# Performance work log

Hardware: AMD Instinct MI355X
Metric: run time of the kernel (lower is better)

Reference implementation:

```python
import jax, jax.numpy as jnp
import numpy as np

L, H, DK, DV, DM, DH = 6, 12, 64, 64, 768, 3072
B, T = 8, 1024


def pos_embed(T, N, dtype):
    pos = jnp.arange(T, dtype=jnp.float32)[:, None]
    i = jnp.arange(N)[None, :]
    exp = ((i // 2) * 2).astype(jnp.float32) / N
    ang = pos / jnp.power(jnp.float32(10000.0), exp)
    pe = jnp.where(i % 2 == 0, jnp.sin(ang), jnp.cos(ang))
    return pe.astype(dtype)


def layernorm(x, g, b, eps=1e-5):
    mu = jnp.mean(x, axis=-1, keepdims=True)
    var = jnp.mean((x - mu) ** 2, axis=-1, keepdims=True)
    return (x - mu) * jax.lax.rsqrt(var + eps) * g + b


def setup_inputs() -> dict:
    key = jax.random.key(0)
    ks = jax.random.split(key, 16)
    s = 0.02
    return {
        "x": jax.random.normal(ks[0], (B, T, DM), dtype=jnp.float32),
        "mask": jnp.ones((B, T), dtype=bool),
        "wq": jax.random.normal(ks[1], (L, H, DM, DK), dtype=jnp.float32) * s,
        "wk": jax.random.normal(ks[2], (L, H, DM, DK), dtype=jnp.float32) * s,
        "wv": jax.random.normal(ks[3], (L, H, DM, DV), dtype=jnp.float32) * s,
        "proj_w": jax.random.normal(ks[4], (L, H * DV, DM), dtype=jnp.float32) * s,
        "proj_b": jnp.zeros((L, DM), dtype=jnp.float32),
        "ln1_g": jnp.ones((L, DM), dtype=jnp.float32),
        "ln1_b": jnp.zeros((L, DM), dtype=jnp.float32),
        "w1": jax.random.normal(ks[5], (L, DM, DH), dtype=jnp.float32) * s,
        "b1": jnp.zeros((L, DH), dtype=jnp.float32),
        "w2": jax.random.normal(ks[6], (L, DH, DM), dtype=jnp.float32) * s,
        "b2": jnp.zeros((L, DM), dtype=jnp.float32),
        "ln2_g": jnp.ones((L, DM), dtype=jnp.float32),
        "ln2_b": jnp.zeros((L, DM), dtype=jnp.float32),
    }


def reference(x, mask, wq, wk, wv, proj_w, proj_b, ln1_g, ln1_b, w1, b1, w2, b2, ln2_g, ln2_b):
    Bx, Tx, Dm = x.shape
    nlayers = wq.shape[0]
    x = x + pos_embed(Tx, Dm, x.dtype)  # sinusoidal PE, added in-place in original
    m = mask[:, None, None, :]          # [B,1,1,Tk], broadcast over heads and queries
    scale = Dm ** 0.5                   # NOTE: original divides by sqrt(Dm), not sqrt(Dk)
    for l in range(nlayers):
        q = jnp.einsum('btd,hdk->bhtk', x, wq[l])
        k = jnp.einsum('bsd,hdk->bhsk', x, wk[l])
        v = jnp.einsum('bsd,hdv->bhsv', x, wv[l])
        attn = jnp.einsum('bhtk,bhsk->bhts', q, k) / scale
        attn = jnp.where(m, attn, -jnp.inf)
        p = jax.nn.softmax(attn, axis=-1)
        o = jnp.einsum('bhts,bhsv->bhtv', p, v)
        o = o.transpose(0, 2, 1, 3).reshape(Bx, Tx, -1)  # concat heads: [B,T,H*Dv]
        o = o @ proj_w[l] + proj_b[l]
        x = layernorm(o + x, ln1_g[l], ln1_b[l])
        h = jax.nn.relu(x @ w1[l] + b1[l])
        f = h @ w2[l] + b2[l]
        x = layernorm(f + x, ln2_g[l], ln2_b[l])
    return x
```

## Files before the change

### kernel.cpp

```cpp
#include <hip/hip_runtime.h>
#include <hip/hip_bf16.h>
#include <math.h>

constexpr int LAYERS = 6;
constexpr int HEADS  = 12;
constexpr int DK     = 64;
constexpr int DM     = 768;
constexpr int DH     = 3072;
constexpr int BATCH  = 8;
constexpr int SEQ    = 1024;
constexpr int MROWS  = BATCH * SEQ;
constexpr float QSCALE = 0.03608439182435161f * 1.4426950408889634f;

typedef __attribute__((ext_vector_type(4))) float f32x4;
typedef __attribute__((ext_vector_type(8))) short bf16x8;
typedef __attribute__((ext_vector_type(4))) unsigned short u16x4;

enum { EPI_QKV = 0, EPI_PROJ = 1, EPI_RELU = 2, EPI_FFN2 = 3 };

__device__ __forceinline__ void gload_lds16(const void* g, void* l) {
  __builtin_amdgcn_global_load_lds(
      (const __attribute__((address_space(1))) void*)g,
      (__attribute__((address_space(3))) void*)l, 16, 0, 0);
}

__global__ __launch_bounds__(256) void posembed_kernel(
    const float* __restrict__ x, float* __restrict__ x_cur,
    __hip_bfloat16* __restrict__ xb) {
  int idx = blockIdx.x * 256 + threadIdx.x;
  int d  = idx % DM;
  int bt = idx / DM;
  int t  = bt & (SEQ - 1);
  float expo = (float)(d & ~1) * (1.0f / (float)DM);
  float inv  = powf(10000.0f, -expo);
  float ang  = (float)t * inv;
  float pe   = (d & 1) ? cosf(ang) : sinf(ang);
  float v = x[idx] + pe;
  x_cur[idx] = v;
  xb[idx] = __float2bfloat16(v);
}

__global__ __launch_bounds__(256) void transpose_conv(
    const float* __restrict__ in, __hip_bfloat16* __restrict__ out,
    int R, int C, long obatch) {
  __shared__ float tile[32][33];
  int batch = blockIdx.z;
  in  += (long)batch * R * C;
  out += (long)batch * obatch;
  int c0 = blockIdx.x * 32, r0 = blockIdx.y * 32;
  int tx = threadIdx.x, ty = threadIdx.y;
  for (int i = 0; i < 4; i++) {
    int r = r0 + ty + i * 8;
    tile[ty + i * 8][tx] = in[(long)r * C + c0 + tx];
  }
  __syncthreads();
  for (int i = 0; i < 4; i++) {
    int oc = ty + i * 8;
    out[(long)(c0 + oc) * R + r0 + tx] = __float2bfloat16(tile[tx][oc]);
  }
}

__global__ __launch_bounds__(256) void qkv_transpose(
    const float* __restrict__ wq, const float* __restrict__ wk,
    const float* __restrict__ wv, __hip_bfloat16* __restrict__ out) {
  __shared__ float tile[32][33];
  const int z = blockIdx.z;
  const int which = z / 12, head = z % 12;
  const float* in = (which == 0 ? wq : which == 1 ? wk : wv)
                    + (size_t)head * DM * DK;
  __hip_bfloat16* o = out + (size_t)which * DM * DM + (size_t)head * DK * DM;
  int c0 = blockIdx.x * 32, r0 = blockIdx.y * 32;
  int tx = threadIdx.x, ty = threadIdx.y;
  for (int i = 0; i < 4; i++) {
    int r = r0 + ty + i * 8;
    tile[ty + i * 8][tx] = in[(long)r * DK + c0 + tx];
  }
  __syncthreads();
  for (int i = 0; i < 4; i++) {
    int oc = ty + i * 8;
    o[(long)(c0 + oc) * DM + r0 + tx] = __float2bfloat16(tile[tx][oc]);
  }
}

__global__ __launch_bounds__(256) void vtrans_kernel(
    const __hip_bfloat16* __restrict__ v, __hip_bfloat16* __restrict__ vt) {
  __shared__ unsigned short tile[64][66];
  const int head = blockIdx.y;
  const int t0 = blockIdx.x * 64;
  const unsigned short* src =
      (const unsigned short*)v + (size_t)head * SEQ * DK + (size_t)t0 * DK;
  unsigned short* dst = (unsigned short*)vt + (size_t)head * SEQ * DK + t0;
  const int tid = threadIdx.x;
#pragma unroll
  for (int it = 0; it < 4; ++it) {
    int j = tid + it * 256;
    int r = j >> 4;
    int c4 = (j & 15) * 4;
    u16x4 d4 = *(const u16x4*)&src[(size_t)r * DK + c4];
    tile[r][c4 + 0] = d4[0]; tile[r][c4 + 1] = d4[1];
    tile[r][c4 + 2] = d4[2]; tile[r][c4 + 3] = d4[3];
  }
  __syncthreads();
#pragma unroll
  for (int it = 0; it < 4; ++it) {
    int j = tid + it * 256;
    int d = j >> 4;
    int t4 = (j & 15) * 4;
    u16x4 o4;
    o4[0] = tile[t4 + 0][d]; o4[1] = tile[t4 + 1][d];
    o4[2] = tile[t4 + 2][d]; o4[3] = tile[t4 + 3][d];
    *(u16x4*)&dst[(size_t)d * SEQ + t4] = o4;
  }
}

template <int EPI>
__global__ __launch_bounds__(256, 2) void gemm_bt(
    const __hip_bfloat16* __restrict__ A,
    const __hip_bfloat16* __restrict__ BT,
    int K,
    const float* __restrict__ bias,
    const float* __restrict__ res,
    void* __restrict__ outp) {
  __shared__ __align__(16) __hip_bfloat16 As[128 * 32];
  __shared__ __align__(16) __hip_bfloat16 Bs[128 * 32];
  const int m0 = blockIdx.y * 128;
  const int n0 = blockIdx.x * 128;
  const int tid = threadIdx.x;
  const int lane = tid & 63;
  const int w = tid >> 6;
  const int wm = w >> 1, wn = w & 1;
  const int g = lane >> 4, r16 = lane & 15;

  f32x4 acc[4][4] = {};

  const int srow = tid >> 2;
  const int scol = (tid & 3) * 8;
  const __hip_bfloat16* aS = A + (size_t)(m0 + srow) * K + scol;
  const __hip_bfloat16* bS = BT + (size_t)(n0 + srow) * K + scol;

  for (int k0 = 0; k0 < K; k0 += 32) {
    __syncthreads();
    gload_lds16(aS + k0,          &As[tid * 8]);
    gload_lds16(aS + 64 * K + k0, &As[2048 + tid * 8]);
    gload_lds16(bS + k0,          &Bs[tid * 8]);
    gload_lds16(bS + 64 * K + k0, &Bs[2048 + tid * 8]);
    __syncthreads();

    bf16x8 af[4], bfr[4];
#pragma unroll
    for (int m = 0; m < 4; m++)
      af[m] = *(const bf16x8*)&As[(wm * 64 + m * 16 + r16) * 32 + g * 8];
#pragma unroll
    for (int n = 0; n < 4; n++)
      bfr[n] = *(const bf16x8*)&Bs[(wn * 64 + n * 16 + r16) * 32 + g * 8];
#pragma unroll
    for (int m = 0; m < 4; m++)
#pragma unroll
      for (int n = 0; n < 4; n++)
        acc[m][n] = __builtin_amdgcn_mfma_f32_16x16x32_bf16(
            af[m], bfr[n], acc[m][n], 0, 0, 0);
  }

#pragma unroll
  for (int m = 0; m < 4; m++)
#pragma unroll
    for (int n = 0; n < 4; n++)
#pragma unroll
      for (int r = 0; r < 4; r++) {
        int row = m0 + wm * 64 + m * 16 + g * 4 + r;
        int col = n0 + wn * 64 + n * 16 + r16;
        float v = acc[m][n][r];
        if (EPI == EPI_QKV) {
          int which = (col >= 2 * DM) ? 2 : (col >= DM ? 1 : 0);
          int hc = col - which * DM;
          int h = hc >> 6, dk = hc & 63;
          int b = row >> 10, t = row & (SEQ - 1);
          if (which == 0) v *= QSCALE;
          ((__hip_bfloat16*)outp)[(((size_t)(which * BATCH + b) * HEADS + h) * SEQ + t) * DK + dk] =
              __float2bfloat16(v);
        } else if (EPI == EPI_PROJ || EPI == EPI_FFN2) {
          ((float*)outp)[(size_t)row * DM + col] =
              v + bias[col] + res[(size_t)row * DM + col];
        } else {
          v += bias[col];
          ((__hip_bfloat16*)outp)[(size_t)row * DH + col] =
              __float2bfloat16(v > 0.f ? v : 0.f);
        }
      }
}

__global__ __launch_bounds__(256, 4) void flash_kernel(
    const __hip_bfloat16* __restrict__ qkv,
    const __hip_bfloat16* __restrict__ vt,
    __hip_bfloat16* __restrict__ obuf) {
  __shared__ __align__(16) char KL[2][8192];
  __shared__ __align__(16) char VL[2][8192];
  __shared__ __align__(16) char PsL[4][2048];

  const int bid = blockIdx.x;
  const int qb = bid / 96;
  const int bh = bid % 96;
  const int h = bh % HEADS, b = bh / HEADS;

  const int tid = threadIdx.x, lane = tid & 63, w = tid >> 6;
  const int g = lane >> 4, r16 = lane & 15;
  const int r7 = r16 & 7;

  const size_t headoff = ((size_t)b * HEADS + h) * SEQ * DK;
  const size_t planes = (size_t)BATCH * HEADS * SEQ * DK;
  const __hip_bfloat16* Q  = qkv + headoff;
  const __hip_bfloat16* Kg = qkv + planes + headoff;
  const __hip_bfloat16* Vg = vt + headoff;

  bf16x8 qf[2];
  {
    int qrow = qb * 64 + w * 16 + r16;
    qf[0] = *(const bf16x8*)&Q[(size_t)qrow * DK + g * 8];
    qf[1] = *(const bf16x8*)&Q[(size_t)qrow * DK + 32 + g * 8];
  }

  f32x4 o_acc[4] = {};
  float m_run = -3e38f;
  float lsum[4] = {0.f, 0.f, 0.f, 0.f};

  const int s0j = tid, s1j = tid + 256;
  const int s0r = s0j >> 3, s0c = (s0j & 7) ^ (s0r & 7);
  const int s1r = s1j >> 3, s1c = (s1j & 7) ^ (s1r & 7);

  auto stage = [&](int tt, int d) {
    const int ss = tt * 64;
    gload_lds16(&Kg[(size_t)(ss + s0r) * DK + s0c * 8], &KL[d][s0j * 16]);
    gload_lds16(&Kg[(size_t)(ss + s1r) * DK + s1c * 8], &KL[d][s1j * 16]);
    gload_lds16(&Vg[(size_t)s0r * SEQ + ss + s0c * 8], &VL[d][s0j * 16]);
    gload_lds16(&Vg[(size_t)s1r * SEQ + ss + s1c * 8], &VL[d][s1j * 16]);
  };

  stage(0, 0);
  __syncthreads();

  for (int t = 0; t < SEQ / 64; ++t) {
    const int cur = t & 1;
    if (t < SEQ / 64 - 1) stage(t + 1, cur ^ 1);

    f32x4 s_acc[4] = {};
#pragma unroll
    for (int n = 0; n < 4; ++n) {
      const int R = n * 16 + r16;
      bf16x8 k0 = *(const bf16x8*)&KL[cur][R * 128 + ((g ^ r7) << 4)];
      s_acc[n] = __builtin_amdgcn_mfma_f32_16x16x32_bf16(qf[0], k0, s_acc[n], 0, 0, 0);
      bf16x8 k1 = *(const bf16x8*)&KL[cur][R * 128 + (((4 + g) ^ r7) << 4)];
      s_acc[n] = __builtin_amdgcn_mfma_f32_16x16x32_bf16(qf[1], k1, s_acc[n], 0, 0, 0);
    }

    float mx = -3e38f;
#pragma unroll
    for (int n = 0; n < 4; ++n)
      mx = fmaxf(mx, fmaxf(fmaxf(s_acc[n][0], s_acc[n][1]),
                           fmaxf(s_acc[n][2], s_acc[n][3])));
#pragma unroll
    for (int off = 1; off < 16; off <<= 1) mx = fmaxf(mx, __shfl_xor(mx, off, 64));

    if (__any(mx > m_run + 8.f)) {
      float mnew = fmaxf(m_run, mx);
      float alpha = exp2f(m_run - mnew);
      m_run = mnew;
#pragma unroll
      for (int r = 0; r < 4; ++r) lsum[r] *= alpha;
#pragma unroll
      for (int n = 0; n < 4; ++n)
#pragma unroll
        for (int r = 0; r < 4; ++r) o_acc[n][r] *= alpha;
    }

    char* Pw = &PsL[w][0];
#pragma unroll
    for (int n = 0; n < 4; ++n)
#pragma unroll
      for (int r = 0; r < 4; ++r) {
        float p = exp2f(s_acc[n][r] - m_run);
        lsum[r] += p;
        int trow = g * 4 + r;
        int chunk = n * 2 + (r16 >> 3);
        *(unsigned short*)&Pw[trow * 128 + ((chunk * 16) ^ ((trow & 7) << 4)) + r7 * 2] =
            __bfloat16_as_ushort(__float2bfloat16(p));
      }

    asm volatile("s_waitcnt lgkmcnt(0)" ::: "memory");
    __builtin_amdgcn_s_barrier();
    __builtin_amdgcn_sched_barrier(0);

#pragma unroll
    for (int kk = 0; kk < 2; ++kk) {
      bf16x8 pf = *(const bf16x8*)&Pw[r16 * 128 + (((kk * 4 + g) * 16) ^ (r7 << 4))];
#pragma unroll
      for (int n = 0; n < 4; ++n) {
        bf16x8 vf = *(const bf16x8*)&VL[cur][(n * 16 + r16) * 128 +
                                            (((kk * 4 + g) ^ r7) << 4)];
        o_acc[n] = __builtin_amdgcn_mfma_f32_16x16x32_bf16(pf, vf, o_acc[n], 0, 0, 0);
      }
    }

    asm volatile("s_waitcnt vmcnt(0)" ::: "memory");
    __builtin_amdgcn_s_barrier();
    __builtin_amdgcn_sched_barrier(0);
  }

#pragma unroll
  for (int r = 0; r < 4; ++r)
#pragma unroll
    for (int off = 1; off < 16; off <<= 1) lsum[r] += __shfl_xor(lsum[r], off, 64);
  float rinv[4];
#pragma unroll
  for (int r = 0; r < 4; ++r) rinv[r] = 1.0f / lsum[r];

#pragma unroll
  for (int n = 0; n < 4; ++n)
#pragma unroll
    for (int r = 0; r < 4; ++r) {
      int t = qb * 64 + w * 16 + g * 4 + r;
      int col = h * DK + n * 16 + r16;
      obuf[((size_t)b * SEQ + t) * DM + col] =
          __float2bfloat16(o_acc[n][r] * rinv[r]);
    }
}

__global__ __launch_bounds__(256) void ln_kernel(
    const float* __restrict__ y, const float* __restrict__ gam,
    const float* __restrict__ bet, float* __restrict__ xout,
    __hip_bfloat16* __restrict__ xb) {
  int row = blockIdx.x;
  const float* yr = y + (size_t)row * DM;
  int tid = threadIdx.x;
  float v[3];
  float s1 = 0.f, s2 = 0.f;
#pragma unroll
  for (int i = 0; i < 3; i++) {
    v[i] = yr[tid + i * 256];
    s1 += v[i];
    s2 += v[i] * v[i];
  }
#pragma unroll
  for (int off = 1; off < 64; off <<= 1) {
    s1 += __shfl_xor(s1, off, 64);
    s2 += __shfl_xor(s2, off, 64);
  }
  __shared__ float ps1[4], ps2[4];
  int w = tid >> 6;
  if ((tid & 63) == 0) { ps1[w] = s1; ps2[w] = s2; }
  __syncthreads();
  s1 = ps1[0] + ps1[1] + ps1[2] + ps1[3];
  s2 = ps2[0] + ps2[1] + ps2[2] + ps2[3];
  float mu = s1 * (1.f / DM);
  float var = s2 * (1.f / DM) - mu * mu;
  float rstd = rsqrtf(var + 1e-5f);
#pragma unroll
  for (int i = 0; i < 3; i++) {
    int d = tid + i * 256;
    float o = (v[i] - mu) * rstd * gam[d] + bet[d];
    xout[(size_t)row * DM + d] = o;
    xb[(size_t)row * DM + d] = __float2bfloat16(o);
  }
}

extern "C" void kernel_launch(void* const* d_in, const int* in_sizes, int n_in,
                              void* d_out, int out_size, void* d_ws, size_t ws_size,
                              hipStream_t stream) {
  const float* x_in   = (const float*)d_in[0];
  const float* wq     = (const float*)d_in[2];
  const float* wk     = (const float*)d_in[3];
  const float* wv     = (const float*)d_in[4];
  const float* proj_w = (const float*)d_in[5];
  const float* proj_b = (const float*)d_in[6];
  const float* ln1_g  = (const float*)d_in[7];
  const float* ln1_b  = (const float*)d_in[8];
  const float* w1     = (const float*)d_in[9];
  const float* b1     = (const float*)d_in[10];
  const float* w2     = (const float*)d_in[11];
  const float* b2     = (const float*)d_in[12];
  const float* ln2_g  = (const float*)d_in[13];
  const float* ln2_b  = (const float*)d_in[14];

  size_t off = 0;
  auto alloc = [&](size_t bytes) {
    void* p = (char*)d_ws + off;
    off += (bytes + 255) & ~(size_t)255;
    return p;
  };
  float* x_cur = (float*)alloc((size_t)MROWS * DM * 4);
  __hip_bfloat16* xb    = (__hip_bfloat16*)alloc((size_t)MROWS * DM * 2);
  __hip_bfloat16* qkvb  = (__hip_bfloat16*)alloc((size_t)3 * MROWS * DM * 2);
  __hip_bfloat16* obuf  = (__hip_bfloat16*)alloc((size_t)MROWS * DM * 2);
  float* ybuf  = (float*)alloc((size_t)MROWS * DM * 4);
  __hip_bfloat16* hbuf  = (__hip_bfloat16*)alloc((size_t)MROWS * DH * 2);
  __hip_bfloat16* qkvt  = (__hip_bfloat16*)alloc((size_t)3 * DM * DM * 2);
  __hip_bfloat16* projt = (__hip_bfloat16*)alloc((size_t)DM * DM * 2);
  __hip_bfloat16* w1t   = (__hip_bfloat16*)alloc((size_t)DH * DM * 2);
  __hip_bfloat16* w2t   = (__hip_bfloat16*)alloc((size_t)DM * DH * 2);
  __hip_bfloat16* vtb   = hbuf;

  posembed_kernel<<<MROWS * DM / 256, 256, 0, stream>>>(x_in, x_cur, xb);

  for (int l = 0; l < LAYERS; l++) {
    qkv_transpose<<<dim3(2, 24, 36), dim3(32, 8), 0, stream>>>(
        wq + (size_t)l * HEADS * DM * DK, wk + (size_t)l * HEADS * DM * DK,
        wv + (size_t)l * HEADS * DM * DK, qkvt);
    transpose_conv<<<dim3(24, 24, 1), dim3(32, 8), 0, stream>>>(
        proj_w + (size_t)l * DM * DM, projt, DM, DM, 0);
    transpose_conv<<<dim3(96, 24, 1), dim3(32, 8), 0, stream>>>(
        w1 + (size_t)l * DM * DH, w1t, DM, DH, 0);
    transpose_conv<<<dim3(24, 96, 1), dim3(32, 8), 0, stream>>>(
        w2 + (size_t)l * DH * DM, w2t, DH, DM, 0);

    gemm_bt<EPI_QKV><<<dim3(18, 64), 256, 0, stream>>>(
        xb, qkvt, DM, nullptr, nullptr, qkvb);
    vtrans_kernel<<<dim3(16, 96), 256, 0, stream>>>(
        qkvb + (size_t)2 * MROWS * DM, vtb);
    flash_kernel<<<dim3((SEQ / 64) * HEADS * BATCH), 256, 0, stream>>>(
        qkvb, vtb, obuf);
    gemm_bt<EPI_PROJ><<<dim3(6, 64), 256, 0, stream>>>(
        obuf, projt, DM, proj_b + (size_t)l * DM, x_cur, ybuf);
    ln_kernel<<<MROWS, 256, 0, stream>>>(
        ybuf, ln1_g + (size_t)l * DM, ln1_b + (size_t)l * DM, x_cur, xb);
    gemm_bt<EPI_RELU><<<dim3(24, 64), 256, 0, stream>>>(
        xb, w1t, DM, b1 + (size_t)l * DH, nullptr, hbuf);
    gemm_bt<EPI_FFN2><<<dim3(6, 64), 256, 0, stream>>>(
        hbuf, w2t, DH, b2 + (size_t)l * DM, x_cur, ybuf);
    float* xo = (l == LAYERS - 1) ? (float*)d_out : x_cur;
    ln_kernel<<<MROWS, 256, 0, stream>>>(
        ybuf, ln2_g + (size_t)l * DM, ln2_b + (size_t)l * DM, xo, xb);
  }
}
```

Before: 1.847 ms.

## Double-buffer GEMM LDS tiles with swizzled layout and MFMA priority boost

The bf16 GEMM mainloop now uses two LDS buffers, so the global-to-LDS load for the next K tile is issued before the MFMAs on the current tile. This overlaps memory latency with compute and needs one barrier per iteration instead of two. The LDS layout is XOR-swizzled to cut bank conflicts on the fragment reads, and s_setprio raises wave priority around the MFMA block. LDS use doubles to 32 KB per block, which could limit occupancy at two blocks per CU.

```diff
diff --git a/kernel.cpp b/kernel.cpp
--- a/kernel.cpp
+++ b/kernel.cpp
@@ -121,8 +121,8 @@
     const float* __restrict__ bias,
     const float* __restrict__ res,
     void* __restrict__ outp) {
-  __shared__ __align__(16) __hip_bfloat16 As[128 * 32];
-  __shared__ __align__(16) __hip_bfloat16 Bs[128 * 32];
+  __shared__ __align__(16) char As[2][8192];
+  __shared__ __align__(16) char Bs[2][8192];
   const int m0 = blockIdx.y * 128;
   const int n0 = blockIdx.x * 128;
   const int tid = threadIdx.x;
@@ -133,32 +133,53 @@
 
   f32x4 acc[4][4] = {};
 
-  const int srow = tid >> 2;
-  const int scol = (tid & 3) * 8;
-  const __hip_bfloat16* aS = A + (size_t)(m0 + srow) * K + scol;
-  const __hip_bfloat16* bS = BT + (size_t)(n0 + srow) * K + scol;
-
-  for (int k0 = 0; k0 < K; k0 += 32) {
-    __syncthreads();
-    gload_lds16(aS + k0,          &As[tid * 8]);
-    gload_lds16(aS + 64 * K + k0, &As[2048 + tid * 8]);
-    gload_lds16(bS + k0,          &Bs[tid * 8]);
-    gload_lds16(bS + 64 * K + k0, &Bs[2048 + tid * 8]);
-    __syncthreads();
+  const int q0 = tid, q1 = tid + 256;
+  const int j0 = q0 >> 3, cc0 = (q0 & 7) ^ (j0 & 7);
+  const int j1 = q1 >> 3, cc1 = (q1 & 7) ^ (j1 & 7);
+  const int mr0 = 2 * j0 + (cc0 >> 2), kc0 = cc0 & 3;
+  const int mr1 = 2 * j1 + (cc1 >> 2), kc1 = cc1 & 3;
+
+  auto stage = [&](int kt, int d) {
+    const int k0 = kt * 32;
+    gload_lds16(&A[(size_t)(m0 + mr0) * K + k0 + kc0 * 8], &As[d][q0 * 16]);
+    gload_lds16(&A[(size_t)(m0 + mr1) * K + k0 + kc1 * 8], &As[d][q1 * 16]);
+    gload_lds16(&BT[(size_t)(n0 + mr0) * K + k0 + kc0 * 8], &Bs[d][q0 * 16]);
+    gload_lds16(&BT[(size_t)(n0 + mr1) * K + k0 + kc1 * 8], &Bs[d][q1 * 16]);
+  };
+
+  auto lds_off = [&](int R) {
+    return (R >> 1) * 128 + (((((R & 1) << 2) | g) ^ ((R >> 1) & 7)) << 4);
+  };
+
+  const int NT = K >> 5;
+  stage(0, 0);
+  asm volatile("s_waitcnt vmcnt(0)" ::: "memory");
+  __builtin_amdgcn_s_barrier();
+  __builtin_amdgcn_sched_barrier(0);
+
+  for (int kt = 0; kt < NT; ++kt) {
+    const int cur = kt & 1;
+    if (kt + 1 < NT) stage(kt + 1, cur ^ 1);
 
     bf16x8 af[4], bfr[4];
 #pragma unroll
     for (int m = 0; m < 4; m++)
-      af[m] = *(const bf16x8*)&As[(wm * 64 + m * 16 + r16) * 32 + g * 8];
+      af[m] = *(const bf16x8*)&As[cur][lds_off(wm * 64 + m * 16 + r16)];
 #pragma unroll
     for (int n = 0; n < 4; n++)
-      bfr[n] = *(const bf16x8*)&Bs[(wn * 64 + n * 16 + r16) * 32 + g * 8];
+      bfr[n] = *(const bf16x8*)&Bs[cur][lds_off(wn * 64 + n * 16 + r16)];
+    __builtin_amdgcn_s_setprio(1);
 #pragma unroll
     for (int m = 0; m < 4; m++)
 #pragma unroll
       for (int n = 0; n < 4; n++)
         acc[m][n] = __builtin_amdgcn_mfma_f32_16x16x32_bf16(
             af[m], bfr[n], acc[m][n], 0, 0, 0);
+    __builtin_amdgcn_s_setprio(0);
+
+    asm volatile("s_waitcnt vmcnt(0)" ::: "memory");
+    __builtin_amdgcn_s_barrier();
+    __builtin_amdgcn_sched_barrier(0);
   }
 
 #pragma unroll
```

Result: no change. 1.830 ms (-0.9%).
